# Kernel tuning notes

Measured on AMD Instinct MI355X. Metric: run time of the kernel, lower is better.

## Reference

```python
import jax, jax.numpy as jnp
import numpy as np

B, T, R = 128, 20, 49           # batch, caption length, num regions (7x7)
V, E, H, FD, A = 10000, 512, 512, 512, 256  # vocab, embed, hidden, feature, attn dims


def setup_inputs() -> dict:
    key = jax.random.key(0)
    ks = jax.random.split(key, 16)
    s = 0.02
    return {
        "features": jax.random.normal(ks[0], (B, R, FD), dtype=jnp.float32),
        "captions": jax.random.randint(ks[1], (B, T), 0, V),
        "emb": jax.random.normal(ks[2], (V, E), dtype=jnp.float32) * s,
        "W_h": jax.random.normal(ks[3], (A, H), dtype=jnp.float32) * s,
        "b_h": jnp.zeros((A,), jnp.float32),
        "W_f": jax.random.normal(ks[4], (A, FD), dtype=jnp.float32) * s,
        "b_f": jnp.zeros((A,), jnp.float32),
        "v_w": jax.random.normal(ks[5], (A,), dtype=jnp.float32) * s,
        "v_b": jnp.zeros((), jnp.float32),
        "W_ih": jax.random.normal(ks[6], (4 * H, E + FD), dtype=jnp.float32) * s,
        "W_hh": jax.random.normal(ks[7], (4 * H, H), dtype=jnp.float32) * s,
        "b_ih": jnp.zeros((4 * H,), jnp.float32),
        "b_hh": jnp.zeros((4 * H,), jnp.float32),
        "fc_W": jax.random.normal(ks[8], (V, H), dtype=jnp.float32) * s,
        "fc_b": jnp.zeros((V,), jnp.float32),
    }


def reference(features, captions, emb, W_h, b_h, W_f, b_f, v_w, v_b,
              W_ih, W_hh, b_ih, b_hh, fc_W, fc_b):
    Bn = features.shape[0]
    Hd = W_hh.shape[1]
    # features are constant across timesteps -> project once (same math as per-step W_f(features))
    f_proj = jnp.einsum('brf,af->bra', features, W_f) + b_f  # (B,R,A)
    embeds = emb[captions[:, :-1]]                            # (B,T-1,E)
    xs = jnp.swapaxes(embeds, 0, 1)                           # (T-1,B,E)
    bias = b_ih + b_hh

    def step(carry, x_t):
        hx, cx = carry
        # Bahdanau attention
        h = hx @ W_h.T + b_h                                  # (B,A)
        scores = jnp.tanh(h[:, None, :] + f_proj) @ v_w + v_b  # (B,R)
        alpha = jax.nn.softmax(scores, axis=1)
        context = jnp.einsum('br,brf->bf', alpha, features)   # (B,FD)
        # LSTMCell (PyTorch gate order: i,f,g,o)
        lstm_in = jnp.concatenate([x_t, context], axis=1)     # (B,E+FD)
        gates = lstm_in @ W_ih.T + hx @ W_hh.T + bias         # (B,4H)
        i, f, g, o = jnp.split(gates, 4, axis=1)
        cx = jax.nn.sigmoid(f) * cx + jax.nn.sigmoid(i) * jnp.tanh(g)
        hx = jax.nn.sigmoid(o) * jnp.tanh(cx)
        logit = hx @ fc_W.T + fc_b                            # (B,V)
        return (hx, cx), logit

    init = (jnp.zeros((Bn, Hd), features.dtype), jnp.zeros((Bn, Hd), features.dtype))
    _, logits = jax.lax.scan(step, init, xs)                  # (T-1,B,V)
    return jnp.swapaxes(logits, 0, 1)                         # (B,T-1,V)
```

## Files before the change

### kernel.cpp

```cpp
#include <hip/hip_runtime.h>
#include <hip/hip_bf16.h>
#include <math.h>

#define NB 128
#define NT 20
#define NS 19
#define NR 49
#define NV 10000
#define NE 512
#define NH 512
#define NFD 512
#define NA 256
#define NG 2048
#define NKC 1536

typedef __bf16 bf16_t;
typedef bf16_t bf16x8 __attribute__((ext_vector_type(8)));
typedef float f32x4 __attribute__((ext_vector_type(4)));

__global__ __launch_bounds__(256) void k_setup(
    const float* __restrict__ W_ih, const float* __restrict__ W_hh,
    const float* __restrict__ b_ih, const float* __restrict__ b_hh,
    const float* __restrict__ W_h, const float* __restrict__ fc_W,
    const float* __restrict__ W_f, const float* __restrict__ features,
    bf16_t* __restrict__ Wcatb, bf16_t* __restrict__ fcWb,
    bf16_t* __restrict__ Wfb, bf16_t* __restrict__ featb,
    float* __restrict__ bias, float* __restrict__ W_hT,
    float* __restrict__ hx, float* __restrict__ cx, bf16_t* __restrict__ hxb)
{
    int idx = blockIdx.x * 256 + threadIdx.x;
    if (idx < NV * NH) fcWb[idx] = (bf16_t)fc_W[idx];
    if (idx < NG * NKC) {
        int n = idx / NKC, k = idx % NKC;
        Wcatb[idx] = (bf16_t)((k < NE + NFD) ? W_ih[n * (NE + NFD) + k]
                                             : W_hh[n * NH + (k - NE - NFD)]);
    }
    if (idx < NB * NR * NFD) featb[idx] = (bf16_t)features[idx];
    if (idx < NA * NFD) Wfb[idx] = (bf16_t)W_f[idx];
    if (idx < NG) bias[idx] = b_ih[idx] + b_hh[idx];
    if (idx < NH * NA) {
        int k = idx / NA, a = idx % NA;
        W_hT[idx] = W_h[a * NH + k];
    }
    if (idx < NB * NH) { hx[idx] = 0.f; cx[idx] = 0.f; hxb[idx] = (bf16_t)0.f; }
}

__global__ __launch_bounds__(1024) void k_attn(
    const float* __restrict__ hx, const float* __restrict__ W_hT,
    const float* __restrict__ b_h, const float* __restrict__ fproj,
    const float* __restrict__ v_w, const float* __restrict__ features,
    const float* __restrict__ emb, const int* __restrict__ captions,
    bf16_t* __restrict__ lin, int t)
{
    int b = blockIdx.x;
    int tid = threadIdx.x;
    __shared__ float hxs[NH];
    __shared__ float part[4][NA];
    __shared__ float hatt[NA];
    __shared__ float salpha[64];

    if (tid < NH) hxs[tid] = hx[b * NH + tid];
    __syncthreads();

    {
        int a = tid & (NA - 1), q = tid >> 8;
        float p = 0.f;
        int k0 = q * (NH / 4);
        #pragma unroll 8
        for (int k = k0; k < k0 + NH / 4; ++k)
            p += hxs[k] * W_hT[k * NA + a];
        part[q][a] = p;
    }
    __syncthreads();
    if (tid < NA)
        hatt[tid] = part[0][tid] + part[1][tid] + part[2][tid] + part[3][tid] + b_h[tid];
    __syncthreads();

    {
        int wv = tid >> 6, lane = tid & 63;
        for (int r = wv; r < NR; r += 16) {
            float s = 0.f;
            const float* fp = fproj + (size_t)(b * NR + r) * NA;
            #pragma unroll
            for (int j = 0; j < 4; ++j) {
                int aa = lane + 64 * j;
                s += tanhf(hatt[aa] + fp[aa]) * v_w[aa];
            }
            #pragma unroll
            for (int off = 32; off; off >>= 1) s += __shfl_xor(s, off);
            if (lane == 0) salpha[r] = s;
        }
    }
    __syncthreads();

    if (tid < 64) {
        float v = (tid < NR) ? salpha[tid] : -INFINITY;
        float m = v;
        #pragma unroll
        for (int off = 32; off; off >>= 1) m = fmaxf(m, __shfl_xor(m, off));
        float e = (tid < NR) ? expf(v - m) : 0.f;
        float ssum = e;
        #pragma unroll
        for (int off = 32; off; off >>= 1) ssum += __shfl_xor(ssum, off);
        if (tid < NR) salpha[tid] = e / ssum;
    }
    __syncthreads();

    if (tid < NH) {
        bf16_t* lrow = lin + (size_t)b * NKC;
        lrow[tid] = (bf16_t)emb[(size_t)captions[b * NT + t] * NE + tid];
        lrow[NE + NFD + tid] = (bf16_t)hxs[tid];
        float c = 0.f;
        #pragma unroll 7
        for (int r = 0; r < NR; ++r)
            c += salpha[r] * features[(size_t)(b * NR + r) * NFD + tid];
        lrow[NE + tid] = (bf16_t)c;
    }
}

__global__ __launch_bounds__(256) void gemm_bf16_nt(
    const bf16_t* __restrict__ Am, const bf16_t* __restrict__ Bm,
    const float* __restrict__ bias, float* __restrict__ Cm,
    int M, int N, int K, int kspan, int ldc, long long zstride)
{
    __shared__ uint4 AsU[512];
    __shared__ uint4 BsU[512];
    int tid = threadIdx.x;
    int m0 = blockIdx.x * 64, n0 = blockIdx.y * 64;
    int k0 = blockIdx.z * kspan;
    int nk = kspan >> 6;

    int rowS = tid >> 3;
    int slotS = tid & 7;
    int wr0 = rowS * 8 + (slotS ^ (rowS & 7));
    int rowS2 = rowS + 32;
    int wr1 = rowS2 * 8 + (slotS ^ (rowS2 & 7));

    const uint4* pA = (const uint4*)(Am + (size_t)(m0 + rowS) * K + k0) + slotS;
    size_t aStep = (size_t)4 * K;
    int nrow0 = n0 + rowS, nrow1 = n0 + rowS2;
    bool bv0 = nrow0 < N, bv1 = nrow1 < N;
    const uint4* pB0 = (const uint4*)(Bm + (size_t)nrow0 * K + k0) + slotS;
    const uint4* pB1 = (const uint4*)(Bm + (size_t)nrow1 * K + k0) + slotS;
    uint4 zz = make_uint4(0, 0, 0, 0);

    int w = tid >> 6, lane = tid & 63;
    int wm = w >> 1, wn = w & 1;
    int lr = lane & 15, lg = lane >> 4;
    int ra[2][2], rb[2][2];
    #pragma unroll
    for (int i = 0; i < 2; ++i)
        #pragma unroll
        for (int kk = 0; kk < 2; ++kk) {
            int rA = wm * 32 + i * 16 + lr;
            int rB = wn * 32 + i * 16 + lr;
            int s = kk * 4 + lg;
            ra[i][kk] = rA * 8 + (s ^ (rA & 7));
            rb[i][kk] = rB * 8 + (s ^ (rB & 7));
        }

    f32x4 acc00 = {}, acc01 = {}, acc10 = {}, acc11 = {};

    uint4 a0 = pA[0], a1 = pA[aStep];
    uint4 b0 = bv0 ? pB0[0] : zz;
    uint4 b1 = bv1 ? pB1[0] : zz;
    pA += 8; pB0 += 8; pB1 += 8;

    for (int kt = 0; kt < nk; ++kt) {
        __syncthreads();
        AsU[wr0] = a0; AsU[wr1] = a1;
        BsU[wr0] = b0; BsU[wr1] = b1;
        if (kt + 1 < nk) {
            a0 = pA[0]; a1 = pA[aStep];
            b0 = bv0 ? pB0[0] : zz;
            b1 = bv1 ? pB1[0] : zz;
            pA += 8; pB0 += 8; pB1 += 8;
        }
        __syncthreads();
        const bf16x8* Af = (const bf16x8*)AsU;
        const bf16x8* Bf = (const bf16x8*)BsU;
        #pragma unroll
        for (int kk = 0; kk < 2; ++kk) {
            bf16x8 fa0 = Af[ra[0][kk]], fa1 = Af[ra[1][kk]];
            bf16x8 fb0 = Bf[rb[0][kk]], fb1 = Bf[rb[1][kk]];
            acc00 = __builtin_amdgcn_mfma_f32_16x16x32_bf16(fa0, fb0, acc00, 0, 0, 0);
            acc01 = __builtin_amdgcn_mfma_f32_16x16x32_bf16(fa0, fb1, acc01, 0, 0, 0);
            acc10 = __builtin_amdgcn_mfma_f32_16x16x32_bf16(fa1, fb0, acc10, 0, 0, 0);
            acc11 = __builtin_amdgcn_mfma_f32_16x16x32_bf16(fa1, fb1, acc11, 0, 0, 0);
        }
    }

    Cm += (size_t)blockIdx.z * zstride;
    f32x4 av[2][2] = {{acc00, acc01}, {acc10, acc11}};
    #pragma unroll
    for (int i = 0; i < 2; ++i) {
        int mbase = m0 + wm * 32 + i * 16 + lg * 4;
        #pragma unroll
        for (int j = 0; j < 2; ++j) {
            int n = n0 + wn * 32 + j * 16 + lr;
            if (n < N) {
                float bz = bias ? bias[n] : 0.f;
                #pragma unroll
                for (int r = 0; r < 4; ++r)
                    Cm[(size_t)(mbase + r) * ldc + n] = av[i][j][r] + bz;
            }
        }
    }
}

__global__ __launch_bounds__(256) void k_lstm(
    const float* __restrict__ gpart, const float* __restrict__ bias,
    float* __restrict__ hx, float* __restrict__ cx, bf16_t* __restrict__ hxb)
{
    int idx = blockIdx.x * 256 + threadIdx.x;
    int b = idx >> 9, h = idx & (NH - 1);
    const float* g0 = gpart + (size_t)b * NG;
    float gi = bias[h],      gf = bias[NH + h];
    float gg = bias[2 * NH + h], go = bias[3 * NH + h];
    #pragma unroll
    for (int z = 0; z < 4; ++z) {
        const float* gz = g0 + (size_t)z * NB * NG;
        gi += gz[h];
        gf += gz[NH + h];
        gg += gz[2 * NH + h];
        go += gz[3 * NH + h];
    }
    float si = 1.f / (1.f + expf(-gi));
    float sf = 1.f / (1.f + expf(-gf));
    float so = 1.f / (1.f + expf(-go));
    float c  = sf * cx[idx] + si * tanhf(gg);
    float hn = so * tanhf(c);
    cx[idx] = c;
    hx[idx] = hn;
    hxb[idx] = (bf16_t)hn;
}

extern "C" void kernel_launch(void* const* d_in, const int* in_sizes, int n_in,
                              void* d_out, int out_size, void* d_ws, size_t ws_size,
                              hipStream_t stream)
{
    const float* features = (const float*)d_in[0];
    const int*   captions = (const int*)d_in[1];
    const float* emb      = (const float*)d_in[2];
    const float* W_h      = (const float*)d_in[3];
    const float* b_h      = (const float*)d_in[4];
    const float* W_f      = (const float*)d_in[5];
    const float* b_f      = (const float*)d_in[6];
    const float* v_w      = (const float*)d_in[7];
    const float* W_ih     = (const float*)d_in[9];
    const float* W_hh     = (const float*)d_in[10];
    const float* b_ih     = (const float*)d_in[11];
    const float* b_hh     = (const float*)d_in[12];
    const float* fc_W     = (const float*)d_in[13];
    const float* fc_b     = (const float*)d_in[14];
    float* out = (float*)d_out;

    char* base = (char*)d_ws;
    bf16_t* Wcatb = (bf16_t*)base;  base += (size_t)NG * NKC * 2;
    bf16_t* fcWb  = (bf16_t*)base;  base += (size_t)NV * NH * 2;
    bf16_t* Wfb   = (bf16_t*)base;  base += (size_t)NA * NFD * 2;
    bf16_t* featb = (bf16_t*)base;  base += (size_t)NB * NR * NFD * 2;
    bf16_t* lin   = (bf16_t*)base;  base += (size_t)NB * NKC * 2;
    bf16_t* hxb   = (bf16_t*)base;  base += (size_t)NB * NH * 2;
    float* bias   = (float*)base;   base += (size_t)NG * 4;
    float* W_hT   = (float*)base;   base += (size_t)NH * NA * 4;
    float* fproj  = (float*)base;   base += (size_t)NB * NR * NA * 4;
    float* hx     = (float*)base;   base += (size_t)NB * NH * 4;
    float* cx     = (float*)base;   base += (size_t)NB * NH * 4;
    float* gpart  = (float*)base;   base += (size_t)4 * NB * NG * 4;

    k_setup<<<dim3((NV * NH + 255) / 256), 256, 0, stream>>>(
        W_ih, W_hh, b_ih, b_hh, W_h, fc_W, W_f, features,
        Wcatb, fcWb, Wfb, featb, bias, W_hT, hx, cx, hxb);

    gemm_bf16_nt<<<dim3(98, 4, 1), 256, 0, stream>>>(
        featb, Wfb, b_f, fproj, NB * NR, NA, NFD, NFD, NA, 0);

    for (int t = 0; t < NS; ++t) {
        k_attn<<<dim3(NB), 1024, 0, stream>>>(
            hx, W_hT, b_h, fproj, v_w, features, emb, captions, lin, t);
        gemm_bf16_nt<<<dim3(2, 32, 4), 256, 0, stream>>>(
            lin, Wcatb, nullptr, gpart, NB, NG, NKC, NKC / 4, NG,
            (long long)NB * NG);
        k_lstm<<<dim3((NB * NH) / 256), 256, 0, stream>>>(gpart, bias, hx, cx, hxb);
        gemm_bf16_nt<<<dim3(2, 157, 1), 256, 0, stream>>>(
            hxb, fcWb, fc_b, out + (size_t)t * NV, NB, NV, NH, NH, NS * NV, 0);
    }
}
```

Baseline: 671.3 us.

## Fuse gate GEMM with LSTM cell and batch all logits into one GEMM

Interleaves the gate rows of the concatenated weights so each 64-column GEMM tile holds complete i/f/g/o quadruples. The LSTM update can then run in the GEMM epilogue, which removes the split-K partial buffer and the separate LSTM kernel. Hidden states for every step are saved, and the per-step vocab projection becomes a single large GEMM after the loop, which removes 19 small launches and reuses fc weights better. Attention now reads bf16 W_h and bf16 features to cut bandwidth. The trade-off is that the gate GEMM loses its split-K parallelism (64 blocks with a longer K loop) and accuracy drops slightly.

```diff
diff --git a/kernel.cpp b/kernel.cpp
--- a/kernel.cpp
+++ b/kernel.cpp
@@ -18,6 +18,8 @@
 typedef bf16_t bf16x8 __attribute__((ext_vector_type(8)));
 typedef float f32x4 __attribute__((ext_vector_type(4)));
 
+__device__ __forceinline__ float sigm(float x) { return 1.f / (1.f + expf(-x)); }
+
 __global__ __launch_bounds__(256) void k_setup(
     const float* __restrict__ W_ih, const float* __restrict__ W_hh,
     const float* __restrict__ b_ih, const float* __restrict__ b_hh,
@@ -25,30 +27,33 @@
     const float* __restrict__ W_f, const float* __restrict__ features,
     bf16_t* __restrict__ Wcatb, bf16_t* __restrict__ fcWb,
     bf16_t* __restrict__ Wfb, bf16_t* __restrict__ featb,
-    float* __restrict__ bias, float* __restrict__ W_hT,
-    float* __restrict__ hx, float* __restrict__ cx, bf16_t* __restrict__ hxb)
+    bf16_t* __restrict__ W_hb, float* __restrict__ bias,
+    float* __restrict__ hx, float* __restrict__ cx)
 {
     int idx = blockIdx.x * 256 + threadIdx.x;
     if (idx < NV * NH) fcWb[idx] = (bf16_t)fc_W[idx];
     if (idx < NG * NKC) {
         int n = idx / NKC, k = idx % NKC;
-        Wcatb[idx] = (bf16_t)((k < NE + NFD) ? W_ih[n * (NE + NFD) + k]
-                                             : W_hh[n * NH + (k - NE - NFD)]);
+        int h = n >> 2, g = n & 3;
+        int orig = g * NH + h;
+        Wcatb[idx] = (bf16_t)((k < NE + NFD) ? W_ih[orig * (NE + NFD) + k]
+                                             : W_hh[orig * NH + (k - NE - NFD)]);
     }
     if (idx < NB * NR * NFD) featb[idx] = (bf16_t)features[idx];
     if (idx < NA * NFD) Wfb[idx] = (bf16_t)W_f[idx];
-    if (idx < NG) bias[idx] = b_ih[idx] + b_hh[idx];
-    if (idx < NH * NA) {
-        int k = idx / NA, a = idx % NA;
-        W_hT[idx] = W_h[a * NH + k];
-    }
-    if (idx < NB * NH) { hx[idx] = 0.f; cx[idx] = 0.f; hxb[idx] = (bf16_t)0.f; }
+    if (idx < NA * NH) W_hb[idx] = (bf16_t)W_h[idx];
+    if (idx < NG) {
+        int h = idx >> 2, g = idx & 3;
+        int orig = g * NH + h;
+        bias[idx] = b_ih[orig] + b_hh[orig];
+    }
+    if (idx < NB * NH) { hx[idx] = 0.f; cx[idx] = 0.f; }
 }
 
 __global__ __launch_bounds__(1024) void k_attn(
-    const float* __restrict__ hx, const float* __restrict__ W_hT,
+    const float* __restrict__ hx, const bf16_t* __restrict__ W_hb,
     const float* __restrict__ b_h, const float* __restrict__ fproj,
-    const float* __restrict__ v_w, const float* __restrict__ features,
+    const float* __restrict__ v_w, const bf16_t* __restrict__ featb,
     const float* __restrict__ emb, const int* __restrict__ captions,
     bf16_t* __restrict__ lin, int t)
 {
@@ -64,11 +69,18 @@
 
     {
         int a = tid & (NA - 1), q = tid >> 8;
+        const bf16x8* wrow = (const bf16x8*)(W_hb + (size_t)a * NH + q * 128);
+        const float* hq = hxs + q * 128;
         float p = 0.f;
-        int k0 = q * (NH / 4);
-        #pragma unroll 8
-        for (int k = k0; k < k0 + NH / 4; ++k)
-            p += hxs[k] * W_hT[k * NA + a];
+        #pragma unroll
+        for (int c = 0; c < 16; ++c) {
+            bf16x8 wv = wrow[c];
+            int k = c * 8;
+            p += hq[k+0]*(float)wv[0] + hq[k+1]*(float)wv[1]
+               + hq[k+2]*(float)wv[2] + hq[k+3]*(float)wv[3]
+               + hq[k+4]*(float)wv[4] + hq[k+5]*(float)wv[5]
+               + hq[k+6]*(float)wv[6] + hq[k+7]*(float)wv[7];
+        }
         part[q][a] = p;
     }
     __syncthreads();
@@ -113,7 +125,7 @@
         float c = 0.f;
         #pragma unroll 7
         for (int r = 0; r < NR; ++r)
-            c += salpha[r] * features[(size_t)(b * NR + r) * NFD + tid];
+            c += salpha[r] * (float)featb[(size_t)(b * NR + r) * NFD + tid];
         lrow[NE + tid] = (bf16_t)c;
     }
 }
@@ -121,27 +133,25 @@
 __global__ __launch_bounds__(256) void gemm_bf16_nt(
     const bf16_t* __restrict__ Am, const bf16_t* __restrict__ Bm,
     const float* __restrict__ bias, float* __restrict__ Cm,
-    int M, int N, int K, int kspan, int ldc, long long zstride)
+    int M, int N, int K, int ldc)
 {
     __shared__ uint4 AsU[512];
     __shared__ uint4 BsU[512];
     int tid = threadIdx.x;
     int m0 = blockIdx.x * 64, n0 = blockIdx.y * 64;
-    int k0 = blockIdx.z * kspan;
-    int nk = kspan >> 6;
-
-    int rowS = tid >> 3;
-    int slotS = tid & 7;
+    int nk = K >> 6;
+
+    int rowS = tid >> 3, slotS = tid & 7;
     int wr0 = rowS * 8 + (slotS ^ (rowS & 7));
     int rowS2 = rowS + 32;
     int wr1 = rowS2 * 8 + (slotS ^ (rowS2 & 7));
 
-    const uint4* pA = (const uint4*)(Am + (size_t)(m0 + rowS) * K + k0) + slotS;
+    const uint4* pA = (const uint4*)(Am + (size_t)(m0 + rowS) * K) + slotS;
     size_t aStep = (size_t)4 * K;
     int nrow0 = n0 + rowS, nrow1 = n0 + rowS2;
     bool bv0 = nrow0 < N, bv1 = nrow1 < N;
-    const uint4* pB0 = (const uint4*)(Bm + (size_t)nrow0 * K + k0) + slotS;
-    const uint4* pB1 = (const uint4*)(Bm + (size_t)nrow1 * K + k0) + slotS;
+    const uint4* pB0 = (const uint4*)(Bm + (size_t)nrow0 * K) + slotS;
+    const uint4* pB1 = (const uint4*)(Bm + (size_t)nrow1 * K) + slotS;
     uint4 zz = make_uint4(0, 0, 0, 0);
 
     int w = tid >> 6, lane = tid & 63;
@@ -160,7 +170,6 @@
         }
 
     f32x4 acc00 = {}, acc01 = {}, acc10 = {}, acc11 = {};
-
     uint4 a0 = pA[0], a1 = pA[aStep];
     uint4 b0 = bv0 ? pB0[0] : zz;
     uint4 b1 = bv1 ? pB1[0] : zz;
@@ -190,7 +199,6 @@
         }
     }
 
-    Cm += (size_t)blockIdx.z * zstride;
     f32x4 av[2][2] = {{acc00, acc01}, {acc10, acc11}};
     #pragma unroll
     for (int i = 0; i < 2; ++i) {
@@ -208,31 +216,194 @@
     }
 }
 
-__global__ __launch_bounds__(256) void k_lstm(
-    const float* __restrict__ gpart, const float* __restrict__ bias,
-    float* __restrict__ hx, float* __restrict__ cx, bf16_t* __restrict__ hxb)
-{
-    int idx = blockIdx.x * 256 + threadIdx.x;
-    int b = idx >> 9, h = idx & (NH - 1);
-    const float* g0 = gpart + (size_t)b * NG;
-    float gi = bias[h],      gf = bias[NH + h];
-    float gg = bias[2 * NH + h], go = bias[3 * NH + h];
-    #pragma unroll
-    for (int z = 0; z < 4; ++z) {
-        const float* gz = g0 + (size_t)z * NB * NG;
-        gi += gz[h];
-        gf += gz[NH + h];
-        gg += gz[2 * NH + h];
-        go += gz[3 * NH + h];
-    }
-    float si = 1.f / (1.f + expf(-gi));
-    float sf = 1.f / (1.f + expf(-gf));
-    float so = 1.f / (1.f + expf(-go));
-    float c  = sf * cx[idx] + si * tanhf(gg);
-    float hn = so * tanhf(c);
-    cx[idx] = c;
-    hx[idx] = hn;
-    hxb[idx] = (bf16_t)hn;
+__global__ __launch_bounds__(256) void k_step(
+    const bf16_t* __restrict__ lin, const bf16_t* __restrict__ Wcatb,
+    const float* __restrict__ bias, float* __restrict__ hx,
+    float* __restrict__ cx, bf16_t* __restrict__ hxAll, int t)
+{
+    __shared__ __align__(16) char smem[16640];
+    uint4* AsU = (uint4*)smem;
+    uint4* BsU = AsU + 512;
+
+    int tid = threadIdx.x;
+    int m0 = blockIdx.x * 64, n0 = blockIdx.y * 64;
+
+    int rowS = tid >> 3, slotS = tid & 7;
+    int wr0 = rowS * 8 + (slotS ^ (rowS & 7));
+    int rowS2 = rowS + 32;
+    int wr1 = rowS2 * 8 + (slotS ^ (rowS2 & 7));
+
+    const uint4* pA = (const uint4*)(lin + (size_t)(m0 + rowS) * NKC) + slotS;
+    const uint4* pB0 = (const uint4*)(Wcatb + (size_t)(n0 + rowS) * NKC) + slotS;
+    const uint4* pB1 = (const uint4*)(Wcatb + (size_t)(n0 + rowS2) * NKC) + slotS;
+    size_t aStep = (size_t)4 * NKC;
+
+    int w = tid >> 6, lane = tid & 63;
+    int wm = w >> 1, wn = w & 1;
+    int lr = lane & 15, lg = lane >> 4;
+    int ra[2][2], rb[2][2];
+    #pragma unroll
+    for (int i = 0; i < 2; ++i)
+        #pragma unroll
+        for (int kk = 0; kk < 2; ++kk) {
+            int rA = wm * 32 + i * 16 + lr;
+            int rB = wn * 32 + i * 16 + lr;
+            int s = kk * 4 + lg;
+            ra[i][kk] = rA * 8 + (s ^ (rA & 7));
+            rb[i][kk] = rB * 8 + (s ^ (rB & 7));
+        }
+
+    f32x4 acc00 = {}, acc01 = {}, acc10 = {}, acc11 = {};
+    uint4 a0 = pA[0], a1 = pA[aStep];
+    uint4 b0 = pB0[0], b1 = pB1[0];
+    pA += 8; pB0 += 8; pB1 += 8;
+
+    #pragma unroll 1
+    for (int kt = 0; kt < NKC / 64; ++kt) {
+        __syncthreads();
+        AsU[wr0] = a0; AsU[wr1] = a1;
+        BsU[wr0] = b0; BsU[wr1] = b1;
+        if (kt + 1 < NKC / 64) {
+            a0 = pA[0]; a1 = pA[aStep];
+            b0 = pB0[0]; b1 = pB1[0];
+            pA += 8; pB0 += 8; pB1 += 8;
+        }
+        __syncthreads();
+        const bf16x8* Af = (const bf16x8*)AsU;
+        const bf16x8* Bf = (const bf16x8*)BsU;
+        #pragma unroll
+        for (int kk = 0; kk < 2; ++kk) {
+            bf16x8 fa0 = Af[ra[0][kk]], fa1 = Af[ra[1][kk]];
+            bf16x8 fb0 = Bf[rb[0][kk]], fb1 = Bf[rb[1][kk]];
+            acc00 = __builtin_amdgcn_mfma_f32_16x16x32_bf16(fa0, fb0, acc00, 0, 0, 0);
+            acc01 = __builtin_amdgcn_mfma_f32_16x16x32_bf16(fa0, fb1, acc01, 0, 0, 0);
+            acc10 = __builtin_amdgcn_mfma_f32_16x16x32_bf16(fa1, fb0, acc10, 0, 0, 0);
+            acc11 = __builtin_amdgcn_mfma_f32_16x16x32_bf16(fa1, fb1, acc11, 0, 0, 0);
+        }
+    }
+
+    __syncthreads();
+    float* Ct = (float*)smem;
+    f32x4 av[2][2] = {{acc00, acc01}, {acc10, acc11}};
+    #pragma unroll
+    for (int i = 0; i < 2; ++i)
+        #pragma unroll
+        for (int j = 0; j < 2; ++j) {
+            int mloc = wm * 32 + i * 16 + lg * 4;
+            int nloc = wn * 32 + j * 16 + lr;
+            #pragma unroll
+            for (int r = 0; r < 4; ++r)
+                Ct[(mloc + r) * 65 + nloc] = av[i][j][r];
+        }
+    __syncthreads();
+
+    int hloc = tid & 15;
+    int h = (n0 >> 2) + hloc;
+    #pragma unroll
+    for (int q = 0; q < 4; ++q) {
+        int m = (tid >> 4) + q * 16;
+        int b = m0 + m;
+        const float* crow = Ct + m * 65 + hloc * 4;
+        const float* brow = bias + n0 + hloc * 4;
+        float gi = crow[0] + brow[0];
+        float gf = crow[1] + brow[1];
+        float gg = crow[2] + brow[2];
+        float go = crow[3] + brow[3];
+        size_t idx = (size_t)b * NH + h;
+        float c = sigm(gf) * cx[idx] + sigm(gi) * tanhf(gg);
+        float hn = sigm(go) * tanhf(c);
+        cx[idx] = c;
+        hx[idx] = hn;
+        hxAll[((size_t)t * NB + b) * NH + h] = (bf16_t)hn;
+    }
+}
+
+__global__ __launch_bounds__(256) void k_logits(
+    const bf16_t* __restrict__ hxAll, const bf16_t* __restrict__ fcWb,
+    const float* __restrict__ fc_b, float* __restrict__ out)
+{
+    __shared__ uint4 AsU[512];
+    __shared__ uint4 BsU[512];
+    int tid = threadIdx.x;
+    int m0 = blockIdx.x * 64, n0 = blockIdx.y * 64;
+
+    int rowS = tid >> 3, slotS = tid & 7;
+    int wr0 = rowS * 8 + (slotS ^ (rowS & 7));
+    int rowS2 = rowS + 32;
+    int wr1 = rowS2 * 8 + (slotS ^ (rowS2 & 7));
+
+    const uint4* pA = (const uint4*)(hxAll + (size_t)(m0 + rowS) * NH) + slotS;
+    size_t aStep = (size_t)4 * NH;
+    int nrow0 = n0 + rowS, nrow1 = n0 + rowS2;
+    bool bv0 = nrow0 < NV, bv1 = nrow1 < NV;
+    const uint4* pB0 = (const uint4*)(fcWb + (size_t)nrow0 * NH) + slotS;
+    const uint4* pB1 = (const uint4*)(fcWb + (size_t)nrow1 * NH) + slotS;
+    uint4 zz = make_uint4(0, 0, 0, 0);
+
+    int w = tid >> 6, lane = tid & 63;
+    int wm = w >> 1, wn = w & 1;
+    int lr = lane & 15, lg = lane >> 4;
+    int ra[2][2], rb[2][2];
+    #pragma unroll
+    for (int i = 0; i < 2; ++i)
+        #pragma unroll
+        for (int kk = 0; kk < 2; ++kk) {
+            int rA = wm * 32 + i * 16 + lr;
+            int rB = wn * 32 + i * 16 + lr;
+            int s = kk * 4 + lg;
+            ra[i][kk] = rA * 8 + (s ^ (rA & 7));
+            rb[i][kk] = rB * 8 + (s ^ (rB & 7));
+        }
+
+    f32x4 acc00 = {}, acc01 = {}, acc10 = {}, acc11 = {};
+    uint4 a0 = pA[0], a1 = pA[aStep];
+    uint4 b0 = bv0 ? pB0[0] : zz;
+    uint4 b1 = bv1 ? pB1[0] : zz;
+    pA += 8; pB0 += 8; pB1 += 8;
+
+    #pragma unroll 1
+    for (int kt = 0; kt < NH / 64; ++kt) {
+        __syncthreads();
+        AsU[wr0] = a0; AsU[wr1] = a1;
+        BsU[wr0] = b0; BsU[wr1] = b1;
+        if (kt + 1 < NH / 64) {
+            a0 = pA[0]; a1 = pA[aStep];
+            b0 = bv0 ? pB0[0] : zz;
+            b1 = bv1 ? pB1[0] : zz;
+            pA += 8; pB0 += 8; pB1 += 8;
+        }
+        __syncthreads();
+        const bf16x8* Af = (const bf16x8*)AsU;
+        const bf16x8* Bf = (const bf16x8*)BsU;
+        #pragma unroll
+        for (int kk = 0; kk < 2; ++kk) {
+            bf16x8 fa0 = Af[ra[0][kk]], fa1 = Af[ra[1][kk]];
+            bf16x8 fb0 = Bf[rb[0][kk]], fb1 = Bf[rb[1][kk]];
+            acc00 = __builtin_amdgcn_mfma_f32_16x16x32_bf16(fa0, fb0, acc00, 0, 0, 0);
+            acc01 = __builtin_amdgcn_mfma_f32_16x16x32_bf16(fa0, fb1, acc01, 0, 0, 0);
+            acc10 = __builtin_amdgcn_mfma_f32_16x16x32_bf16(fa1, fb0, acc10, 0, 0, 0);
+            acc11 = __builtin_amdgcn_mfma_f32_16x16x32_bf16(fa1, fb1, acc11, 0, 0, 0);
+        }
+    }
+
+    f32x4 av[2][2] = {{acc00, acc01}, {acc10, acc11}};
+    #pragma unroll
+    for (int i = 0; i < 2; ++i) {
+        int mbase = m0 + wm * 32 + i * 16 + lg * 4;
+        #pragma unroll
+        for (int j = 0; j < 2; ++j) {
+            int n = n0 + wn * 32 + j * 16 + lr;
+            if (n < NV) {
+                float bz = fc_b[n];
+                #pragma unroll
+                for (int r = 0; r < 4; ++r) {
+                    int m = mbase + r;
+                    int b = m & 127, tt = m >> 7;
+                    out[((size_t)b * NS + tt) * NV + n] = av[i][j][r] + bz;
+                }
+            }
+        }
+    }
 }
 
 extern "C" void kernel_launch(void* const* d_in, const int* in_sizes, int n_in,
@@ -261,29 +432,26 @@
     bf16_t* Wfb   = (bf16_t*)base;  base += (size_t)NA * NFD * 2;
     bf16_t* featb = (bf16_t*)base;  base += (size_t)NB * NR * NFD * 2;
     bf16_t* lin   = (bf16_t*)base;  base += (size_t)NB * NKC * 2;
-    bf16_t* hxb   = (bf16_t*)base;  base += (size_t)NB * NH * 2;
+    bf16_t* W_hb  = (bf16_t*)base;  base += (size_t)NA * NH * 2;
+    bf16_t* hxAll = (bf16_t*)base;  base += (size_t)NS * NB * NH * 2;
     float* bias   = (float*)base;   base += (size_t)NG * 4;
-    float* W_hT   = (float*)base;   base += (size_t)NH * NA * 4;
     float* fproj  = (float*)base;   base += (size_t)NB * NR * NA * 4;
     float* hx     = (float*)base;   base += (size_t)NB * NH * 4;
     float* cx     = (float*)base;   base += (size_t)NB * NH * 4;
-    float* gpart  = (float*)base;   base += (size_t)4 * NB * NG * 4;
 
     k_setup<<<dim3((NV * NH + 255) / 256), 256, 0, stream>>>(
         W_ih, W_hh, b_ih, b_hh, W_h, fc_W, W_f, features,
-        Wcatb, fcWb, Wfb, featb, bias, W_hT, hx, cx, hxb);
-
-    gemm_bf16_nt<<<dim3(98, 4, 1), 256, 0, stream>>>(
-        featb, Wfb, b_f, fproj, NB * NR, NA, NFD, NFD, NA, 0);
+        Wcatb, fcWb, Wfb, featb, W_hb, bias, hx, cx);
+
+    gemm_bf16_nt<<<dim3(98, 4), 256, 0, stream>>>(
+        featb, Wfb, b_f, fproj, NB * NR, NA, NFD, NA);
 
     for (int t = 0; t < NS; ++t) {
         k_attn<<<dim3(NB), 1024, 0, stream>>>(
-            hx, W_hT, b_h, fproj, v_w, features, emb, captions, lin, t);
-        gemm_bf16_nt<<<dim3(2, 32, 4), 256, 0, stream>>>(
-            lin, Wcatb, nullptr, gpart, NB, NG, NKC, NKC / 4, NG,
-            (long long)NB * NG);
-        k_lstm<<<dim3((NB * NH) / 256), 256, 0, stream>>>(gpart, bias, hx, cx, hxb);
-        gemm_bf16_nt<<<dim3(2, 157, 1), 256, 0, stream>>>(
-            hxb, fcWb, fc_b, out + (size_t)t * NV, NB, NV, NH, NH, NS * NV, 0);
-    }
-}
+            hx, W_hb, b_h, fproj, v_w, featb, emb, captions, lin, t);
+        k_step<<<dim3(2, 32), 256, 0, stream>>>(
+            lin, Wcatb, bias, hx, cx, hxAll, t);
+    }
+
+    k_logits<<<dim3(38, 157), 256, 0, stream>>>(hxAll, fcWb, fc_b, out);
+}
```

New measurement: 682.5 us. About the same (+1.7%).
